# Performance work log

Hardware: AMD Instinct MI355X
Metric: run time of the kernel (lower is better)

The kernel has to match this reference:

```python
import jax, jax.numpy as jnp
import numpy as np

WS = 8
NH = 8
C = 192
HD = C // NH
SCALE = HD ** -0.5
EPS = 1e-5


def setup_inputs() -> dict:
    key = jax.random.key(0)
    ks = jax.random.split(key, 7)
    B, H, W = 8, 256, 256
    x = jax.random.normal(ks[0], (B, C, H, W), dtype=jnp.float32)
    gamma = jnp.ones((C,), dtype=jnp.float32)
    beta = jnp.zeros((C,), dtype=jnp.float32)
    w_qkv = jax.random.normal(ks[1], (C, 3 * C), dtype=jnp.float32) * (C ** -0.5)
    b_qkv = jnp.zeros((3 * C,), dtype=jnp.float32)
    w_proj = jax.random.normal(ks[2], (C, C), dtype=jnp.float32) * (C ** -0.5)
    b_proj = jnp.zeros((C,), dtype=jnp.float32)
    return {"x": x, "gamma": gamma, "beta": beta, "w_qkv": w_qkv,
            "b_qkv": b_qkv, "w_proj": w_proj, "b_proj": b_proj}


def reference(x, gamma, beta, w_qkv, b_qkv, w_proj, b_proj):
    B, Cc, H, W = x.shape
    # H, W chosen divisible by WS -> pad branch is a no-op
    nh, nw = H // WS, W // WS
    # window partition: [B,C,H,W] -> [B*nh*nw, WS*WS, C]
    xw = x.reshape(B, Cc, nh, WS, nw, WS)
    xw = xw.transpose(0, 2, 4, 3, 5, 1).reshape(-1, WS * WS, Cc)
    # LayerNorm over channel dim
    mu = xw.mean(axis=-1, keepdims=True)
    var = jnp.mean((xw - mu) ** 2, axis=-1, keepdims=True)
    xn = (xw - mu) * jax.lax.rsqrt(var + EPS) * gamma + beta
    # QKV projection -> [3, nWin, NH, S, HD]
    S = WS * WS
    qkv = (xn @ w_qkv + b_qkv).reshape(-1, S, 3, NH, HD)
    qkv = qkv.transpose(2, 0, 3, 1, 4)
    q, k, v = qkv[0], qkv[1], qkv[2]
    attn = jax.nn.softmax(jnp.einsum('whsd,whtd->whst', q, k) * SCALE, axis=-1)
    xa = jnp.einsum('whst,whtd->whsd', attn, v)
    xa = xa.transpose(0, 2, 1, 3).reshape(-1, S, Cc)
    xa = xa @ w_proj + b_proj
    # un-window: -> [B, C, H, W]
    xa = xa.reshape(B, nh, nw, WS, WS, Cc)
    xa = xa.transpose(0, 5, 1, 3, 2, 4).reshape(B, Cc, H, W)
    return jax.nn.sigmoid(xa.mean(axis=1, keepdims=True))
```

## Files before the change

### kernel.cpp

```cpp
#include <hip/hip_runtime.h>
#include <hip/hip_bf16.h>


typedef __attribute__((ext_vector_type(4))) float floatx4;
typedef __attribute__((ext_vector_type(8))) short short8;

#define SCALE_Q 0.20412414523193154f
#define LN_EPS 1e-5f

#define RXN 200
#define RQK 264
#define RPC 40
#define OFF_XN    0
#define OFF_Q     25600
#define OFF_K     59392
#define OFF_PC    93184
#define OFF_LOGIT 134144
#define OFF_VW    134400
#define LDS_BYTES 136448

__device__ __forceinline__ floatx4 mfma16(short8 a, short8 b, floatx4 c) {
  return __builtin_amdgcn_mfma_f32_16x16x32_bf16(a, b, c, 0, 0, 0);
}

__global__ void prep_kernel(const float* __restrict__ w_qkv,
                            const float* __restrict__ w_proj,
                            const float* __restrict__ b_proj,
                            __hip_bfloat16* __restrict__ wfrag,
                            float* __restrict__ wbar) {
  int tid = blockIdx.x * 256 + threadIdx.x;
  if (tid < 36 * 6 * 64) {
    int j = tid / 384, rem = tid % 384, ksr = rem / 64, l = rem % 64;
    int n  = 16 * j + (l & 15);
    int k0 = 32 * ksr + (l >> 4) * 8;
#pragma unroll
    for (int i = 0; i < 8; ++i)
      wfrag[(size_t)tid * 8 + i] = __float2bfloat16(w_qkv[(k0 + i) * 576 + n]);
  }
  if (tid < 192) {
    float s = 0.f;
    for (int c = 0; c < 192; ++c) s += w_proj[tid * 192 + c];
    wbar[tid] = s * (1.f / 192.f);
  } else if (tid == 192) {
    float s = 0.f;
    for (int c = 0; c < 192; ++c) s += b_proj[c];
    wbar[192] = s * (1.f / 192.f);
  }
}

__global__ __launch_bounds__(512, 2) void swin_kernel(
    const float* __restrict__ x,
    const float* __restrict__ gamma,
    const float* __restrict__ beta,
    const float* __restrict__ b_qkv,
    const __hip_bfloat16* __restrict__ wfrag,
    const float* __restrict__ wbar,
    float* __restrict__ out) {
  __shared__ __align__(16) char smem[LDS_BYTES];
  __hip_bfloat16* xn = (__hip_bfloat16*)(smem + OFF_XN);
  __hip_bfloat16* lq = (__hip_bfloat16*)(smem + OFF_Q);
  __hip_bfloat16* lk = (__hip_bfloat16*)(smem + OFF_K);
  float* logit = (float*)(smem + OFF_LOGIT);
  float* vwf   = (float*)(smem + OFF_VW);
  float2* scratch = (float2*)(smem + OFF_PC);

  const int tid = threadIdx.x;
  const int w   = tid >> 6;
  const int l   = tid & 63;
  const int l15 = l & 15;
  const int lg  = l >> 4;
  __hip_bfloat16* pcw = (__hip_bfloat16*)(smem + OFF_PC + w * (64 * RPC * 2));
  const floatx4 fzero = {0.f, 0.f, 0.f, 0.f};

  for (int i = tid; i < 64 * 64; i += 512) {
    int rr = i >> 6, hc = i & 63;
    int hh = hc >> 3, dd = 24 + (hc & 7);
    lq[rr * RQK + hh * 32 + dd] = __float2bfloat16(0.f);
    lk[rr * RQK + hh * 32 + dd] = __float2bfloat16(0.f);
  }
  if (tid < 64) logit[tid] = 0.f;
  vwf[tid] = 0.f;
  __syncthreads();

  const int p  = blockIdx.x;
  const int bb = p & 7;
  const int wh = p >> 3;
  const int tr = l >> 3, tc = l & 7;
  const int c0 = w * 24;
  const float* xb = x + (size_t)bb * 192 * 65536 + (size_t)(wh * 8 + tr) * 256 + tc;

  float xr[24];
#pragma unroll
  for (int i = 0; i < 24; ++i) xr[i] = xb[(size_t)(c0 + i) * 65536];

#pragma unroll 1
  for (int it = 0; it < 32; ++it) {
    float s1 = 0.f, s2 = 0.f;
#pragma unroll
    for (int i = 0; i < 24; ++i) { s1 += xr[i]; s2 += xr[i] * xr[i]; }
    scratch[w * 64 + l] = make_float2(s1, s2);
    __syncthreads();
    float ts = 0.f, tq = 0.f;
#pragma unroll
    for (int g = 0; g < 8; ++g) { float2 v = scratch[g * 64 + l]; ts += v.x; tq += v.y; }
    const float mu   = ts * (1.f / 192.f);
    const float rstd = rsqrtf(tq * (1.f / 192.f) - mu * mu + LN_EPS);
#pragma unroll
    for (int i = 0; i < 24; ++i) {
      float xv = (xr[i] - mu) * rstd * gamma[c0 + i] + beta[c0 + i];
      xn[l * RXN + c0 + i] = __float2bfloat16(xv);
    }
    __syncthreads();

    if (it < 31) {
#pragma unroll
      for (int i = 0; i < 24; ++i)
        xr[i] = xb[(size_t)(c0 + i) * 65536 + (it + 1) * 8];
    }

    short8 af[4][6];
#pragma unroll
    for (int mi = 0; mi < 4; ++mi)
#pragma unroll
      for (int ks = 0; ks < 6; ++ks)
        af[mi][ks] = *(const short8*)&xn[(16 * mi + l15) * RXN + 32 * ks + lg * 8];

    for (int j = w; j < 36; j += 8) {
      floatx4 aa[4];
#pragma unroll
      for (int mi = 0; mi < 4; ++mi) aa[mi] = fzero;
      const short8* bp = (const short8*)wfrag + (size_t)(j * 384 + l);
#pragma unroll
      for (int ks = 0; ks < 6; ++ks) {
        short8 bf = bp[ks * 64];
#pragma unroll
        for (int mi = 0; mi < 4; ++mi) aa[mi] = mfma16(af[mi][ks], bf, aa[mi]);
      }
      const int n = 16 * j + l15;
      const float bias = b_qkv[n];
      if (j < 12) {
        const int hh = n / 24, dd = n - hh * 24;
#pragma unroll
        for (int mi = 0; mi < 4; ++mi)
#pragma unroll
          for (int rg = 0; rg < 4; ++rg) {
            int t = 16 * mi + lg * 4 + rg;
            lq[t * RQK + hh * 32 + dd] = __float2bfloat16((aa[mi][rg] + bias) * SCALE_Q);
          }
      } else if (j < 24) {
        const int cc = n - 192;
        const int hh = cc / 24, dd = cc - hh * 24;
#pragma unroll
        for (int mi = 0; mi < 4; ++mi)
#pragma unroll
          for (int rg = 0; rg < 4; ++rg) {
            int t = 16 * mi + lg * 4 + rg;
            lk[t * RQK + hh * 32 + dd] = __float2bfloat16(aa[mi][rg] + bias);
          }
      } else {
        const int cc = n - 384;
        const int hh = cc / 24;
        const float wbv = wbar[cc];
        float part[16];
#pragma unroll
        for (int mi = 0; mi < 4; ++mi)
#pragma unroll
          for (int rg = 0; rg < 4; ++rg)
            part[mi * 4 + rg] = (aa[mi][rg] + bias) * wbv;
#pragma unroll
        for (int v2 = 0; v2 < 16; ++v2) {
          float t0 = part[v2];
          t0 += __shfl_xor(t0, 1);
          t0 += __shfl_xor(t0, 2);
          t0 += __shfl_xor(t0, 4);
          part[v2] = t0;
        }
        if ((l15 & 7) == 0) {
#pragma unroll
          for (int mi = 0; mi < 4; ++mi)
#pragma unroll
            for (int rg = 0; rg < 4; ++rg) {
              int t = 16 * mi + lg * 4 + rg;
              atomicAdd(&vwf[hh * 64 + t], part[mi * 4 + rg]);
            }
        }
      }
    }
    __syncthreads();

    {
      const int hh = w;
      short8 qf[4], kf[4];
#pragma unroll
      for (int i = 0; i < 4; ++i) {
        qf[i] = *(const short8*)&lq[(16 * i + l15) * RQK + hh * 32 + lg * 8];
        kf[i] = *(const short8*)&lk[(16 * i + l15) * RQK + hh * 32 + lg * 8];
      }
      floatx4 sc[4][4];
#pragma unroll
      for (int i = 0; i < 4; ++i)
#pragma unroll
        for (int j2 = 0; j2 < 4; ++j2)
          sc[i][j2] = mfma16(qf[i], kf[j2], fzero);
#pragma unroll
      for (int i = 0; i < 4; ++i)
#pragma unroll
        for (int j2 = 0; j2 < 4; ++j2)
#pragma unroll
          for (int rg = 0; rg < 4; ++rg)
            sc[i][j2][rg] = exp2f(sc[i][j2][rg] * 1.44269504f);

      short8 vwfrag[2], onesf;
#pragma unroll
      for (int q2 = 0; q2 < 8; ++q2) onesf[q2] = (short)0x3F80;
#pragma unroll
      for (int kc = 0; kc < 2; ++kc)
#pragma unroll
        for (int q2 = 0; q2 < 8; ++q2) {
          __hip_bfloat16 hb = __float2bfloat16(vwf[hh * 64 + kc * 32 + lg * 8 + q2]);
          short sv; __builtin_memcpy(&sv, &hb, 2);
          vwfrag[kc][q2] = sv;
        }

      floatx4 cacc[4], racc[4];
#pragma unroll
      for (int i = 0; i < 4; ++i) { cacc[i] = fzero; racc[i] = fzero; }
#pragma unroll
      for (int kc = 0; kc < 2; ++kc) {
#pragma unroll
        for (int i = 0; i < 4; ++i)
#pragma unroll
          for (int jj = 0; jj < 2; ++jj)
#pragma unroll
            for (int rg = 0; rg < 4; ++rg) {
              int row = 16 * i + lg * 4 + rg;
              pcw[row * RPC + jj * 16 + l15] = __float2bfloat16(sc[i][kc * 2 + jj][rg]);
            }
#pragma unroll
        for (int i = 0; i < 4; ++i) {
          short8 pf = *(const short8*)&pcw[(16 * i + l15) * RPC + lg * 8];
          cacc[i] = mfma16(pf, vwfrag[kc], cacc[i]);
          racc[i] = mfma16(pf, onesf, racc[i]);
        }
      }
      if (l15 == 0) {
#pragma unroll
        for (int i = 0; i < 4; ++i)
#pragma unroll
          for (int rg = 0; rg < 4; ++rg) {
            int row = 16 * i + lg * 4 + rg;
            atomicAdd(&logit[row], cacc[i][rg] / racc[i][rg]);
          }
      }
    }
    __syncthreads();

    if (tid < 64) {
      float vL = logit[tid] + wbar[192];
      out[(size_t)bb * 65536 + (size_t)(wh * 8 + (tid >> 3)) * 256 + it * 8 + (tid & 7)]
          = 1.f / (1.f + __expf(-vL));
      logit[tid] = 0.f;
    }
    vwf[tid] = 0.f;
  }
}

extern "C" void kernel_launch(void* const* d_in, const int* in_sizes, int n_in,
                              void* d_out, int out_size, void* d_ws, size_t ws_size,
                              hipStream_t stream) {
  const float* x      = (const float*)d_in[0];
  const float* gamma  = (const float*)d_in[1];
  const float* beta   = (const float*)d_in[2];
  const float* w_qkv  = (const float*)d_in[3];
  const float* b_qkv  = (const float*)d_in[4];
  const float* w_proj = (const float*)d_in[5];
  const float* b_proj = (const float*)d_in[6];
  float* out = (float*)d_out;

  __hip_bfloat16* wfrag = (__hip_bfloat16*)d_ws;
  float* wbar = (float*)((char*)d_ws + 221184);

  prep_kernel<<<54, 256, 0, stream>>>(w_qkv, w_proj, b_proj, wfrag, wbar);
  swin_kernel<<<256, 512, 0, stream>>>(x, gamma, beta, b_qkv, wfrag, wbar, out);
}
```

Before: 1.185 ms.

## Shrink LDS by aliasing buffers, split window rows across blocks, drop P·V MFMA

Aliases the normalized-input buffer onto the Q region and the LN scratch onto the K region, and removes the per-wave P staging buffer. This roughly halves LDS per block so more blocks can be resident, and launch bounds are raised to match. Each block now handles half a window row, so the grid doubles to 512 blocks and fills more of the GPU. The probability-times-vw reduction now uses VALU multiply-adds and cross-lane shuffles instead of LDS round-trips and MFMAs. It also adds an extra barrier, re-zeroes the padded head columns every iteration, and moves the next input prefetch later, which may expose more of the load latency.

```diff
diff --git a/kernel.cpp b/kernel.cpp
--- a/kernel.cpp
+++ b/kernel.cpp
@@ -10,14 +10,11 @@
 
 #define RXN 200
 #define RQK 264
-#define RPC 40
-#define OFF_XN    0
-#define OFF_Q     25600
-#define OFF_K     59392
-#define OFF_PC    93184
-#define OFF_LOGIT 134144
-#define OFF_VW    134400
-#define LDS_BYTES 136448
+#define OFF_LQ    0
+#define OFF_LK    33792
+#define OFF_VW    67584
+#define OFF_LOGIT 69632
+#define LDS_BYTES 69888
 
 __device__ __forceinline__ floatx4 mfma16(short8 a, short8 b, floatx4 c) {
   return __builtin_amdgcn_mfma_f32_16x16x32_bf16(a, b, c, 0, 0, 0);
@@ -48,7 +45,7 @@
   }
 }
 
-__global__ __launch_bounds__(512, 2) void swin_kernel(
+__global__ __launch_bounds__(512, 4) void swin_kernel(
     const float* __restrict__ x,
     const float* __restrict__ gamma,
     const float* __restrict__ beta,
@@ -57,44 +54,39 @@
     const float* __restrict__ wbar,
     float* __restrict__ out) {
   __shared__ __align__(16) char smem[LDS_BYTES];
-  __hip_bfloat16* xn = (__hip_bfloat16*)(smem + OFF_XN);
-  __hip_bfloat16* lq = (__hip_bfloat16*)(smem + OFF_Q);
-  __hip_bfloat16* lk = (__hip_bfloat16*)(smem + OFF_K);
+  __hip_bfloat16* lq = (__hip_bfloat16*)(smem + OFF_LQ);
+  __hip_bfloat16* lk = (__hip_bfloat16*)(smem + OFF_LK);
+  __hip_bfloat16* xn = lq;
+  float2* scratch = (float2*)(smem + OFF_LK);
+  float* vwf   = (float*)(smem + OFF_VW);
   float* logit = (float*)(smem + OFF_LOGIT);
-  float* vwf   = (float*)(smem + OFF_VW);
-  float2* scratch = (float2*)(smem + OFF_PC);
 
   const int tid = threadIdx.x;
   const int w   = tid >> 6;
   const int l   = tid & 63;
   const int l15 = l & 15;
   const int lg  = l >> 4;
-  __hip_bfloat16* pcw = (__hip_bfloat16*)(smem + OFF_PC + w * (64 * RPC * 2));
   const floatx4 fzero = {0.f, 0.f, 0.f, 0.f};
-
-  for (int i = tid; i < 64 * 64; i += 512) {
-    int rr = i >> 6, hc = i & 63;
-    int hh = hc >> 3, dd = 24 + (hc & 7);
-    lq[rr * RQK + hh * 32 + dd] = __float2bfloat16(0.f);
-    lk[rr * RQK + hh * 32 + dd] = __float2bfloat16(0.f);
-  }
+  const short8 zero8 = {0, 0, 0, 0, 0, 0, 0, 0};
+
   if (tid < 64) logit[tid] = 0.f;
   vwf[tid] = 0.f;
-  __syncthreads();
-
-  const int p  = blockIdx.x;
-  const int bb = p & 7;
-  const int wh = p >> 3;
+
+  const int p    = blockIdx.x;
+  const int bb   = p & 7;
+  const int wh   = (p >> 3) & 31;
+  const int half = p >> 8;
   const int tr = l >> 3, tc = l & 7;
   const int c0 = w * 24;
-  const float* xb = x + (size_t)bb * 192 * 65536 + (size_t)(wh * 8 + tr) * 256 + tc;
+  const float* xb = x + (size_t)bb * 192 * 65536 + (size_t)(wh * 8 + tr) * 256
+                      + half * 128 + tc;
 
   float xr[24];
 #pragma unroll
   for (int i = 0; i < 24; ++i) xr[i] = xb[(size_t)(c0 + i) * 65536];
 
 #pragma unroll 1
-  for (int it = 0; it < 32; ++it) {
+  for (int it = 0; it < 16; ++it) {
     float s1 = 0.f, s2 = 0.f;
 #pragma unroll
     for (int i = 0; i < 24; ++i) { s1 += xr[i]; s2 += xr[i] * xr[i]; }
@@ -105,18 +97,21 @@
     for (int g = 0; g < 8; ++g) { float2 v = scratch[g * 64 + l]; ts += v.x; tq += v.y; }
     const float mu   = ts * (1.f / 192.f);
     const float rstd = rsqrtf(tq * (1.f / 192.f) - mu * mu + LN_EPS);
-#pragma unroll
-    for (int i = 0; i < 24; ++i) {
-      float xv = (xr[i] - mu) * rstd * gamma[c0 + i] + beta[c0 + i];
-      xn[l * RXN + c0 + i] = __float2bfloat16(xv);
-    }
-    __syncthreads();
-
-    if (it < 31) {
-#pragma unroll
-      for (int i = 0; i < 24; ++i)
-        xr[i] = xb[(size_t)(c0 + i) * 65536 + (it + 1) * 8];
-    }
+    short8 pk[3];
+#pragma unroll
+    for (int ch = 0; ch < 3; ++ch)
+#pragma unroll
+      for (int q2 = 0; q2 < 8; ++q2) {
+        float xv = (xr[ch * 8 + q2] - mu) * rstd * gamma[c0 + ch * 8 + q2]
+                   + beta[c0 + ch * 8 + q2];
+        __hip_bfloat16 hb = __float2bfloat16(xv);
+        short sv; __builtin_memcpy(&sv, &hb, 2);
+        pk[ch][q2] = sv;
+      }
+#pragma unroll
+    for (int ch = 0; ch < 3; ++ch)
+      *(short8*)&xn[l * RXN + c0 + ch * 8] = pk[ch];
+    __syncthreads();
 
     short8 af[4][6];
 #pragma unroll
@@ -124,6 +119,12 @@
 #pragma unroll
       for (int ks = 0; ks < 6; ++ks)
         af[mi][ks] = *(const short8*)&xn[(16 * mi + l15) * RXN + 32 * ks + lg * 8];
+    __syncthreads();
+
+    { int t = tid >> 3, hh = tid & 7;
+      *(short8*)&lq[t * RQK + hh * 32 + 24] = zero8; }
+    if (tid < 64) { int t = tid >> 3, hh = tid & 7;
+      *(short8*)&lk[t * RQK + hh * 32 + 24] = zero8; }
 
     for (int j = w; j < 36; j += 8) {
       floatx4 aa[4];
@@ -189,6 +190,11 @@
     __syncthreads();
 
     {
+      if (it < 15) {
+#pragma unroll
+        for (int i = 0; i < 24; ++i)
+          xr[i] = xb[(size_t)(c0 + i) * 65536 + (it + 1) * 8];
+      }
       const int hh = w;
       short8 qf[4], kf[4];
 #pragma unroll
@@ -210,55 +216,35 @@
           for (int rg = 0; rg < 4; ++rg)
             sc[i][j2][rg] = exp2f(sc[i][j2][rg] * 1.44269504f);
 
-      short8 vwfrag[2], onesf;
-#pragma unroll
-      for (int q2 = 0; q2 < 8; ++q2) onesf[q2] = (short)0x3F80;
-#pragma unroll
-      for (int kc = 0; kc < 2; ++kc)
-#pragma unroll
-        for (int q2 = 0; q2 < 8; ++q2) {
-          __hip_bfloat16 hb = __float2bfloat16(vwf[hh * 64 + kc * 32 + lg * 8 + q2]);
-          short sv; __builtin_memcpy(&sv, &hb, 2);
-          vwfrag[kc][q2] = sv;
+      float vwv[4];
+#pragma unroll
+      for (int j2 = 0; j2 < 4; ++j2) vwv[j2] = vwf[hh * 64 + j2 * 16 + l15];
+
+#pragma unroll
+      for (int i = 0; i < 4; ++i)
+#pragma unroll
+        for (int rg = 0; rg < 4; ++rg) {
+          float d0 = 0.f, s0 = 0.f;
+#pragma unroll
+          for (int j2 = 0; j2 < 4; ++j2) {
+            float pv = sc[i][j2][rg];
+            d0 += pv * vwv[j2];
+            s0 += pv;
+          }
+          d0 += __shfl_xor(d0, 1); s0 += __shfl_xor(s0, 1);
+          d0 += __shfl_xor(d0, 2); s0 += __shfl_xor(s0, 2);
+          d0 += __shfl_xor(d0, 4); s0 += __shfl_xor(s0, 4);
+          d0 += __shfl_xor(d0, 8); s0 += __shfl_xor(s0, 8);
+          if (l15 == 0)
+            atomicAdd(&logit[16 * i + lg * 4 + rg], d0 / s0);
         }
-
-      floatx4 cacc[4], racc[4];
-#pragma unroll
-      for (int i = 0; i < 4; ++i) { cacc[i] = fzero; racc[i] = fzero; }
-#pragma unroll
-      for (int kc = 0; kc < 2; ++kc) {
-#pragma unroll
-        for (int i = 0; i < 4; ++i)
-#pragma unroll
-          for (int jj = 0; jj < 2; ++jj)
-#pragma unroll
-            for (int rg = 0; rg < 4; ++rg) {
-              int row = 16 * i + lg * 4 + rg;
-              pcw[row * RPC + jj * 16 + l15] = __float2bfloat16(sc[i][kc * 2 + jj][rg]);
-            }
-#pragma unroll
-        for (int i = 0; i < 4; ++i) {
-          short8 pf = *(const short8*)&pcw[(16 * i + l15) * RPC + lg * 8];
-          cacc[i] = mfma16(pf, vwfrag[kc], cacc[i]);
-          racc[i] = mfma16(pf, onesf, racc[i]);
-        }
-      }
-      if (l15 == 0) {
-#pragma unroll
-        for (int i = 0; i < 4; ++i)
-#pragma unroll
-          for (int rg = 0; rg < 4; ++rg) {
-            int row = 16 * i + lg * 4 + rg;
-            atomicAdd(&logit[row], cacc[i][rg] / racc[i][rg]);
-          }
-      }
     }
     __syncthreads();
 
     if (tid < 64) {
       float vL = logit[tid] + wbar[192];
-      out[(size_t)bb * 65536 + (size_t)(wh * 8 + (tid >> 3)) * 256 + it * 8 + (tid & 7)]
-          = 1.f / (1.f + __expf(-vL));
+      out[(size_t)bb * 65536 + (size_t)(wh * 8 + (tid >> 3)) * 256
+          + (half * 16 + it) * 8 + (tid & 7)] = 1.f / (1.f + __expf(-vL));
       logit[tid] = 0.f;
     }
     vwf[tid] = 0.f;
@@ -281,5 +267,5 @@
   float* wbar = (float*)((char*)d_ws + 221184);
 
   prep_kernel<<<54, 256, 0, stream>>>(w_qkv, w_proj, b_proj, wfrag, wbar);
-  swin_kernel<<<256, 512, 0, stream>>>(x, gamma, beta, b_qkv, wfrag, wbar, out);
-}
+  swin_kernel<<<512, 512, 0, stream>>>(x, gamma, beta, b_qkv, wfrag, wbar, out);
+}
```

Result: slower. 1.511 ms (+27.5%).
